# Kernel tuning notes

Measured on AMD Instinct MI355X. Metric: run time of the kernel, lower is better.

## Reference

```python
import jax, jax.numpy as jnp
import numpy as np

BUFFER_C = 1.25

def setup_inputs() -> dict:
    key = jax.random.key(0)
    k1, k2, k3 = jax.random.split(key, 3)
    T, D, E = 4096, 1024, 8
    x = jax.random.normal(k1, (T, D), dtype=jnp.float32)
    Wg = jax.random.normal(k2, (D, E), dtype=jnp.float32) / np.sqrt(D)
    bg = jnp.zeros((E,), dtype=jnp.float32)
    W = jax.random.normal(k3, (E, D, D), dtype=jnp.float32) / np.sqrt(D)
    b = jnp.zeros((E, D), dtype=jnp.float32)
    return {"x": x, "Wg": Wg, "bg": bg, "W": W, "b": b}


def reference(x, Wg, bg, W, b):
    # Top-1 (Switch-style) routing with capacity buffer, per-expert Linear,
    # prob-weighted combine, plus load-balancing aux loss.
    T, D = x.shape
    E = W.shape[0]
    capacity = int(BUFFER_C * T / E)

    logits = x @ Wg + bg                      # [T, E]
    probs = jax.nn.softmax(logits, axis=-1)   # [T, E]
    top_idx = jnp.argmax(probs, axis=-1)      # [T]
    top_prob = jnp.take_along_axis(probs, top_idx[:, None], axis=-1)[:, 0]

    onehot = jax.nn.one_hot(top_idx, E, dtype=x.dtype)       # [T, E]
    # 1-indexed position of each token within its expert's buffer
    pos = jnp.cumsum(onehot, axis=0) * onehot                # [T, E]
    dispatch = jnp.where((onehot > 0) & (pos <= capacity), 1.0, 0.0).astype(x.dtype)

    # dense dispatch/combine equivalent of the masked per-expert loop
    xe = jnp.einsum('te,td->etd', dispatch, x)               # [E, T, D]
    ye = jnp.einsum('etd,edf->etf', xe, W) + b[:, None, :]   # [E, T, D]
    y = jnp.einsum('te,etf->tf', dispatch, ye)               # [T, D] (0 for dropped)
    out = y * top_prob[:, None]

    # aux load-balance loss: E * sum_e f_e * P_e
    f = onehot.mean(axis=0)
    P = probs.mean(axis=0)
    aux_loss = E * jnp.sum(f * P)
    return out, aux_loss
```

## Files before the change

### kernel.cpp

```cpp
#include <hip/hip_runtime.h>
#include <hip/hip_bf16.h>
#include <cstdint>

#define T_TOK 4096
#define D_DIM 1024
#define E_EXP 8
#define CAP   640
#define NBIN  64
#define MAXDROP 3456
#define MT    10

typedef __attribute__((ext_vector_type(8))) short short8;
typedef __attribute__((ext_vector_type(4))) float f32x4;

__device__ inline unsigned short f2bf(float f) {
    uint32_t u = __float_as_uint(f);
    u += 0x7fffu + ((u >> 16) & 1u);
    return (unsigned short)(u >> 16);
}

__device__ inline void dma16(const void* g, void* l) {
    __builtin_amdgcn_global_load_lds(
        (const __attribute__((address_space(1))) unsigned int*)g,
        (__attribute__((address_space(3))) unsigned int*)l, 16, 0, 0);
}

#define WB_TILE(e, nt, kt) ((((size_t)(e) * 16 + (nt)) * 16 + (kt)) * 4096)
#define XG_TILE(e, mt, kt) ((((size_t)(e) * MT + (mt)) * 16 + (kt)) * 4096)

__global__ __launch_bounds__(256) void prep_kernel(
    const float* __restrict__ x, const float* __restrict__ Wg,
    const float* __restrict__ bg, const float* __restrict__ W,
    unsigned short* __restrict__ Wb,
    int* __restrict__ top_idx, float* __restrict__ top_prob, float* __restrict__ ppart)
{
    int bid = blockIdx.x;
    int tid = threadIdx.x;

    if (bid < 2048) {
        __shared__ unsigned short tile[64][66];
        int e  = bid >> 8;
        int kt = (bid >> 4) & 15;
        int nt = bid & 15;
        int k0 = kt * 64, n0 = nt * 64;
        const float* Wsrc = W + (size_t)e * D_DIM * D_DIM;
        #pragma unroll
        for (int p = 0; p < 4; p++) {
            int kk = p * 16 + (tid >> 4);
            int nn = (tid & 15) * 4;
            float4 v = *(const float4*)(Wsrc + (size_t)(k0 + kk) * D_DIM + n0 + nn);
            ushort4 u;
            u.x = f2bf(v.x); u.y = f2bf(v.y); u.z = f2bf(v.z); u.w = f2bf(v.w);
            *(ushort4*)&tile[kk][nn] = u;
        }
        __syncthreads();
        unsigned short* dst = Wb + WB_TILE(e, nt, kt);
        #pragma unroll
        for (int p = 0; p < 2; p++) {
            int c = tid + 256 * p;
            int g = c >> 6, n = c & 63;
            short8 v;
            #pragma unroll
            for (int z = 0; z < 8; z++) v[z] = (short)tile[g * 8 + z][n];
            *(short8*)&dst[(size_t)c * 8] = v;
        }
    } else {
        __shared__ float WgT[8][1024];
        #pragma unroll
        for (int r = 0; r < 4; r++) {
            int d = tid + 256 * r;
            const float4* wr = (const float4*)(Wg + (size_t)d * 8);
            float4 a = wr[0], bq = wr[1];
            WgT[0][d] = a.x;  WgT[1][d] = a.y;  WgT[2][d] = a.z;  WgT[3][d] = a.w;
            WgT[4][d] = bq.x; WgT[5][d] = bq.y; WgT[6][d] = bq.z; WgT[7][d] = bq.w;
        }
        __syncthreads();

        int wid  = tid >> 6;
        int lane = tid & 63;
        int t = (bid - 2048) * 4 + wid;

        const float* xr = x + (size_t)t * D_DIM;

        float acc[8];
        #pragma unroll
        for (int e = 0; e < 8; e++) acc[e] = 0.f;

        #pragma unroll
        for (int ii = 0; ii < 8; ii++) {
            int da = lane + 128 * ii;
            int db = da + 64;
            float xa = xr[da];
            float xc = xr[db];
            #pragma unroll
            for (int e = 0; e < 8; e++)
                acc[e] += xa * WgT[e][da] + xc * WgT[e][db];
        }
        #pragma unroll
        for (int off = 32; off > 0; off >>= 1) {
            #pragma unroll
            for (int e = 0; e < 8; e++) acc[e] += __shfl_xor(acc[e], off, 64);
        }
        if (lane == 0) {
            float lg[8];
            #pragma unroll
            for (int e = 0; e < 8; e++) lg[e] = acc[e] + bg[e];
            float m = lg[0]; int am = 0;
            #pragma unroll
            for (int e = 1; e < 8; e++) { if (lg[e] > m) { m = lg[e]; am = e; } }
            float ex[8], s = 0.f;
            #pragma unroll
            for (int e = 0; e < 8; e++) { ex[e] = expf(lg[e] - m); s += ex[e]; }
            float inv = 1.f / s;
            top_idx[t]  = am;
            top_prob[t] = ex[am] * inv;
            int bin = (int)(bid & (NBIN - 1));
            #pragma unroll
            for (int e = 0; e < 8; e++) atomicAdd(&ppart[bin * 8 + e], ex[e] * inv);
        }
    }
}

__global__ __launch_bounds__(1024) void scan_kernel(
    const int* __restrict__ top_idx,
    int* __restrict__ tok_list, int* __restrict__ cnt,
    const float* __restrict__ ppart,
    float* __restrict__ out, float* __restrict__ out_aux)
{
    __shared__ int counts[64][8];
    __shared__ int excl[64][8];
    __shared__ int fulltot[8];
    __shared__ int droplist[MAXDROP];
    __shared__ int ndrop;

    int tid  = threadIdx.x;
    int wv   = tid >> 6;
    int lane = tid & 63;
    unsigned long long ltmask = (lane == 0) ? 0ull : ((~0ull) >> (64 - lane));

    if (tid == 0) ndrop = 0;

    int ecache[4];
    #pragma unroll
    for (int c = 0; c < 4; c++)
        ecache[c] = top_idx[(4 * wv + c) * 64 + lane];

    #pragma unroll
    for (int c = 0; c < 4; c++) {
        int chunk = 4 * wv + c;
        int e = ecache[c];
        #pragma unroll
        for (int q = 0; q < 8; q++) {
            unsigned long long mk = __ballot(e == q);
            int tot = __popcll(mk);
            if (lane == q) counts[chunk][q] = tot;
        }
    }
    __syncthreads();

    if (wv == 0) {
        #pragma unroll
        for (int q = 0; q < 8; q++) {
            int v = counts[lane][q];
            int orig = v;
            #pragma unroll
            for (int off = 1; off < 64; off <<= 1) {
                int n = __shfl_up(v, off, 64);
                if (lane >= off) v += n;
            }
            excl[lane][q] = v - orig;
            int total = __shfl(v, 63, 64);
            if (lane == 0) {
                fulltot[q] = total;
                cnt[q] = total < CAP ? total : CAP;
            }
        }
    }
    __syncthreads();

    #pragma unroll
    for (int c = 0; c < 4; c++) {
        int chunk = 4 * wv + c;
        int t = chunk * 64 + lane;
        int e = ecache[c];
        int pos = 0;
        #pragma unroll
        for (int q = 0; q < 8; q++) {
            unsigned long long mk = __ballot(e == q);
            if (e == q) pos = excl[chunk][q] + __popcll(mk & ltmask);
        }
        if (pos < CAP) {
            tok_list[e * CAP + pos] = t;
        } else {
            int di = atomicAdd(&ndrop, 1);
            droplist[di] = t;
        }
    }
    __syncthreads();

    int nd = ndrop;
    int grp = tid >> 8;
    int col = (tid & 255) * 4;
    float4 z = {0.f, 0.f, 0.f, 0.f};
    for (int d = grp; d < nd; d += 4) {
        int row = droplist[d];
        *(float4*)&out[(size_t)row * D_DIM + col] = z;
    }

    if (wv == 0) {
        float p[8];
        #pragma unroll
        for (int e = 0; e < 8; e++) p[e] = ppart[lane * 8 + e];
        #pragma unroll
        for (int off = 32; off > 0; off >>= 1) {
            #pragma unroll
            for (int e = 0; e < 8; e++) p[e] += __shfl_xor(p[e], off, 64);
        }
        if (lane == 0) {
            float s = 0.f;
            #pragma unroll
            for (int e = 0; e < 8; e++)
                s += ((float)fulltot[e] / (float)T_TOK) * (p[e] / (float)T_TOK);
            out_aux[0] = (float)E_EXP * s;
        }
    }
}

__global__ __launch_bounds__(256) void gather_kernel(
    const float* __restrict__ x, const int* __restrict__ tok_list,
    const int* __restrict__ cnt, unsigned short* __restrict__ xg)
{
    int bid = blockIdx.x;
    int e   = bid / 40;
    int rem = bid % 40;
    int mt  = rem >> 2, ktg = rem & 3;
    int count = cnt[e];
    int m0 = mt * 64;
    if (m0 >= count) return;

    int tid = threadIdx.x;
    const int* tl = tok_list + e * CAP;

    #pragma unroll
    for (int kk = 0; kk < 4; kk++) {
        int kt = ktg * 4 + kk;
        unsigned short* dst = xg + XG_TILE(e, mt, kt);
        #pragma unroll
        for (int p = 0; p < 2; p++) {
            int c = tid + 256 * p;
            int g = c >> 6, row = c & 63;
            int gm = m0 + row;
            int tok = tl[gm < count ? gm : count - 1];
            const float* src = x + (size_t)tok * D_DIM + kt * 64 + g * 8;
            float4 v0 = *(const float4*)(src);
            float4 v1 = *(const float4*)(src + 4);
            short8 v;
            v[0] = f2bf(v0.x); v[1] = f2bf(v0.y); v[2] = f2bf(v0.z); v[3] = f2bf(v0.w);
            v[4] = f2bf(v1.x); v[5] = f2bf(v1.y); v[6] = f2bf(v1.z); v[7] = f2bf(v1.w);
            *(short8*)&dst[(size_t)c * 8] = v;
        }
    }
}

__device__ inline void stage_dma(const unsigned short* gAt, const unsigned short* gBt,
                                 unsigned short (*Ab)[64][8], unsigned short (*Bb)[64][8],
                                 int w, int lane)
{
    size_t lo = (size_t)lane * 8;
    dma16(gAt + (size_t)w * 512 + lo,       &Ab[w][0][0]);
    dma16(gAt + (size_t)(w + 4) * 512 + lo, &Ab[w + 4][0][0]);
    dma16(gBt + (size_t)w * 512 + lo,       &Bb[w][0][0]);
    dma16(gBt + (size_t)(w + 4) * 512 + lo, &Bb[w + 4][0][0]);
}

__global__ __launch_bounds__(256) void expert_gemm(
    const unsigned short* __restrict__ xg, const unsigned short* __restrict__ Wb,
    const float* __restrict__ bias,
    const int* __restrict__ tok_list, const int* __restrict__ cnt,
    const float* __restrict__ top_prob, float* __restrict__ out)
{
    int bid = blockIdx.x;
    int e   = bid / (MT * 16);
    int rem = bid % (MT * 16);
    int mt  = rem >> 4, nt = rem & 15;
    int count = cnt[e];
    int m0 = mt * 64;
    if (m0 >= count) return;
    int n0 = nt * 64;

    __shared__ unsigned short Ab[2][8][64][8];
    __shared__ unsigned short Bb[2][8][64][8];

    int tid  = threadIdx.x;
    int lane = tid & 63, w = tid >> 6;
    int quad = lane >> 4, l16 = lane & 15;
    int mw = (w >> 1) * 32, nw = (w & 1) * 32;

    const int* tl = tok_list + e * CAP;
    const unsigned short* gA0 = xg + XG_TILE(e, mt, 0);
    const unsigned short* gB0 = Wb + WB_TILE(e, nt, 0);

    f32x4 acc[2][2];
    #pragma unroll
    for (int i = 0; i < 2; i++)
        #pragma unroll
        for (int j = 0; j < 2; j++)
            acc[i][j] = (f32x4){0.f, 0.f, 0.f, 0.f};

    stage_dma(gA0, gB0, Ab[0], Bb[0], w, lane);

    int cur = 0;
    #pragma unroll 1
    for (int kt = 0; kt < 16; kt++) {
        __syncthreads();
        if (kt + 1 < 16)
            stage_dma(gA0 + (size_t)(kt + 1) * 4096, gB0 + (size_t)(kt + 1) * 4096,
                      Ab[cur ^ 1], Bb[cur ^ 1], w, lane);

        short8 af[2][2], bf[2][2];
        #pragma unroll
        for (int s = 0; s < 2; s++) {
            #pragma unroll
            for (int i = 0; i < 2; i++) {
                af[s][i] = *(const short8*)&Ab[cur][s * 4 + quad][mw + 16 * i + l16][0];
                bf[s][i] = *(const short8*)&Bb[cur][s * 4 + quad][nw + 16 * i + l16][0];
            }
        }
        #pragma unroll
        for (int s = 0; s < 2; s++)
            #pragma unroll
            for (int i = 0; i < 2; i++)
                #pragma unroll
                for (int j = 0; j < 2; j++)
                    acc[i][j] = __builtin_amdgcn_mfma_f32_16x16x32_bf16(
                        af[s][i], bf[s][j], acc[i][j], 0, 0, 0);
        cur ^= 1;
    }

    float bv[2];
    #pragma unroll
    for (int j = 0; j < 2; j++)
        bv[j] = bias[e * D_DIM + n0 + nw + 16 * j + l16];

    #pragma unroll
    for (int i = 0; i < 2; i++) {
        int rb = m0 + mw + 16 * i + quad * 4;
        #pragma unroll
        for (int r = 0; r < 4; r++) {
            int gm = rb + r;
            if (gm >= count) continue;
            int tok = tl[gm];
            float p = top_prob[tok];
            float* orow = out + (size_t)tok * D_DIM + n0 + nw + l16;
            #pragma unroll
            for (int j = 0; j < 2; j++)
                orow[16 * j] = (acc[i][j][r] + bv[j]) * p;
        }
    }
}

extern "C" void kernel_launch(void* const* d_in, const int* in_sizes, int n_in,
                              void* d_out, int out_size, void* d_ws, size_t ws_size,
                              hipStream_t stream) {
    const float* x  = (const float*)d_in[0];
    const float* Wg = (const float*)d_in[1];
    const float* bg = (const float*)d_in[2];
    const float* W  = (const float*)d_in[3];
    const float* b  = (const float*)d_in[4];
    float* out = (float*)d_out;

    char* ws = (char*)d_ws;
    unsigned short* Wb = (unsigned short*)(ws + 0);
    unsigned short* xg = (unsigned short*)(ws + 16777216);
    int*   top_idx  = (int*)(ws + 27262976);
    float* top_prob = (float*)(ws + 27279360);
    int*   tok_list = (int*)(ws + 27295744);
    int*   cnt      = (int*)(ws + 27316224);
    float* ppart    = (float*)(ws + 27316256);

    hipMemsetAsync(ppart, 0, NBIN * 8 * sizeof(float), stream);
    hipLaunchKernelGGL(prep_kernel, dim3(2048 + T_TOK / 4), dim3(256), 0, stream,
                       x, Wg, bg, W, Wb, top_idx, top_prob, ppart);
    hipLaunchKernelGGL(scan_kernel, dim3(1), dim3(1024), 0, stream,
                       top_idx, tok_list, cnt, ppart, out, out + (size_t)T_TOK * D_DIM);
    hipLaunchKernelGGL(gather_kernel, dim3(320), dim3(256), 0, stream,
                       x, tok_list, cnt, xg);
    hipLaunchKernelGGL(expert_gemm, dim3(E_EXP * MT * 16), dim3(256), 0, stream,
                       xg, Wb, b, tok_list, cnt, top_prob, out);
}
```

Before: 166.9 us.

## Split prep into transpose and gate kernels, widen GEMM M-tile to 128

The fused prep kernel is split into a weight transpose/convert kernel and a separate gate kernel using 1024-thread blocks. The separate memset is dropped and ppart is zeroed inside the transpose kernel instead. The expert GEMM tile grows from 64x64 to 128x64 so each W tile loaded from memory feeds twice as many rows, halving B traffic. The cost is more accumulators per thread and fewer blocks in the grid. Splitting prep also serializes gating after the transpose, where the two halves previously ran concurrently in one launch.

Result: no change. 167.2 us (+0.2%).

```diff
diff --git a/kernel.cpp b/kernel.cpp
--- a/kernel.cpp
+++ b/kernel.cpp
@@ -28,96 +28,96 @@
 #define WB_TILE(e, nt, kt) ((((size_t)(e) * 16 + (nt)) * 16 + (kt)) * 4096)
 #define XG_TILE(e, mt, kt) ((((size_t)(e) * MT + (mt)) * 16 + (kt)) * 4096)
 
-__global__ __launch_bounds__(256) void prep_kernel(
+__global__ __launch_bounds__(256) void trans_kernel(
+    const float* __restrict__ W, unsigned short* __restrict__ Wb,
+    float* __restrict__ ppart)
+{
+    __shared__ unsigned short tile[64][66];
+    int bid = blockIdx.x, tid = threadIdx.x;
+    if (bid == 0) { ppart[tid] = 0.f; ppart[tid + 256] = 0.f; }
+
+    int e  = bid >> 8;
+    int kt = (bid >> 4) & 15;
+    int nt = bid & 15;
+    int k0 = kt * 64, n0 = nt * 64;
+    const float* Wsrc = W + (size_t)e * D_DIM * D_DIM;
+    #pragma unroll
+    for (int p = 0; p < 4; p++) {
+        int kk = p * 16 + (tid >> 4);
+        int nn = (tid & 15) * 4;
+        float4 v = *(const float4*)(Wsrc + (size_t)(k0 + kk) * D_DIM + n0 + nn);
+        ushort4 u;
+        u.x = f2bf(v.x); u.y = f2bf(v.y); u.z = f2bf(v.z); u.w = f2bf(v.w);
+        *(ushort4*)&tile[kk][nn] = u;
+    }
+    __syncthreads();
+    unsigned short* dst = Wb + WB_TILE(e, nt, kt);
+    #pragma unroll
+    for (int p = 0; p < 2; p++) {
+        int c = tid + 256 * p;
+        int g = c >> 6, n = c & 63;
+        short8 v;
+        #pragma unroll
+        for (int z = 0; z < 8; z++) v[z] = (short)tile[g * 8 + z][n];
+        *(short8*)&dst[(size_t)c * 8] = v;
+    }
+}
+
+__global__ __launch_bounds__(1024) void gate_kernel(
     const float* __restrict__ x, const float* __restrict__ Wg,
-    const float* __restrict__ bg, const float* __restrict__ W,
-    unsigned short* __restrict__ Wb,
+    const float* __restrict__ bg,
     int* __restrict__ top_idx, float* __restrict__ top_prob, float* __restrict__ ppart)
 {
-    int bid = blockIdx.x;
+    __shared__ float WgT[8][1024];
     int tid = threadIdx.x;
-
-    if (bid < 2048) {
-        __shared__ unsigned short tile[64][66];
-        int e  = bid >> 8;
-        int kt = (bid >> 4) & 15;
-        int nt = bid & 15;
-        int k0 = kt * 64, n0 = nt * 64;
-        const float* Wsrc = W + (size_t)e * D_DIM * D_DIM;
-        #pragma unroll
-        for (int p = 0; p < 4; p++) {
-            int kk = p * 16 + (tid >> 4);
-            int nn = (tid & 15) * 4;
-            float4 v = *(const float4*)(Wsrc + (size_t)(k0 + kk) * D_DIM + n0 + nn);
-            ushort4 u;
-            u.x = f2bf(v.x); u.y = f2bf(v.y); u.z = f2bf(v.z); u.w = f2bf(v.w);
-            *(ushort4*)&tile[kk][nn] = u;
-        }
-        __syncthreads();
-        unsigned short* dst = Wb + WB_TILE(e, nt, kt);
-        #pragma unroll
-        for (int p = 0; p < 2; p++) {
-            int c = tid + 256 * p;
-            int g = c >> 6, n = c & 63;
-            short8 v;
-            #pragma unroll
-            for (int z = 0; z < 8; z++) v[z] = (short)tile[g * 8 + z][n];
-            *(short8*)&dst[(size_t)c * 8] = v;
-        }
-    } else {
-        __shared__ float WgT[8][1024];
-        #pragma unroll
-        for (int r = 0; r < 4; r++) {
-            int d = tid + 256 * r;
-            const float4* wr = (const float4*)(Wg + (size_t)d * 8);
-            float4 a = wr[0], bq = wr[1];
-            WgT[0][d] = a.x;  WgT[1][d] = a.y;  WgT[2][d] = a.z;  WgT[3][d] = a.w;
-            WgT[4][d] = bq.x; WgT[5][d] = bq.y; WgT[6][d] = bq.z; WgT[7][d] = bq.w;
-        }
-        __syncthreads();
-
-        int wid  = tid >> 6;
-        int lane = tid & 63;
-        int t = (bid - 2048) * 4 + wid;
-
-        const float* xr = x + (size_t)t * D_DIM;
-
-        float acc[8];
-        #pragma unroll
-        for (int e = 0; e < 8; e++) acc[e] = 0.f;
-
-        #pragma unroll
-        for (int ii = 0; ii < 8; ii++) {
-            int da = lane + 128 * ii;
-            int db = da + 64;
-            float xa = xr[da];
-            float xc = xr[db];
-            #pragma unroll
-            for (int e = 0; e < 8; e++)
-                acc[e] += xa * WgT[e][da] + xc * WgT[e][db];
-        }
-        #pragma unroll
-        for (int off = 32; off > 0; off >>= 1) {
-            #pragma unroll
-            for (int e = 0; e < 8; e++) acc[e] += __shfl_xor(acc[e], off, 64);
-        }
-        if (lane == 0) {
-            float lg[8];
-            #pragma unroll
-            for (int e = 0; e < 8; e++) lg[e] = acc[e] + bg[e];
-            float m = lg[0]; int am = 0;
-            #pragma unroll
-            for (int e = 1; e < 8; e++) { if (lg[e] > m) { m = lg[e]; am = e; } }
-            float ex[8], s = 0.f;
-            #pragma unroll
-            for (int e = 0; e < 8; e++) { ex[e] = expf(lg[e] - m); s += ex[e]; }
-            float inv = 1.f / s;
-            top_idx[t]  = am;
-            top_prob[t] = ex[am] * inv;
-            int bin = (int)(bid & (NBIN - 1));
-            #pragma unroll
-            for (int e = 0; e < 8; e++) atomicAdd(&ppart[bin * 8 + e], ex[e] * inv);
-        }
+    {
+        const float4* wr = (const float4*)(Wg + (size_t)tid * 8);
+        float4 a = wr[0], bq = wr[1];
+        WgT[0][tid] = a.x;  WgT[1][tid] = a.y;  WgT[2][tid] = a.z;  WgT[3][tid] = a.w;
+        WgT[4][tid] = bq.x; WgT[5][tid] = bq.y; WgT[6][tid] = bq.z; WgT[7][tid] = bq.w;
+    }
+    __syncthreads();
+
+    int wid  = tid >> 6;
+    int lane = tid & 63;
+    int t = blockIdx.x * 16 + wid;
+
+    const float* xr = x + (size_t)t * D_DIM;
+    float acc[8];
+    #pragma unroll
+    for (int e = 0; e < 8; e++) acc[e] = 0.f;
+
+    #pragma unroll
+    for (int ii = 0; ii < 8; ii++) {
+        int da = lane + 128 * ii;
+        int db = da + 64;
+        float xa = xr[da];
+        float xc = xr[db];
+        #pragma unroll
+        for (int e = 0; e < 8; e++)
+            acc[e] += xa * WgT[e][da] + xc * WgT[e][db];
+    }
+    #pragma unroll
+    for (int off = 32; off > 0; off >>= 1) {
+        #pragma unroll
+        for (int e = 0; e < 8; e++) acc[e] += __shfl_xor(acc[e], off, 64);
+    }
+    if (lane == 0) {
+        float lg[8];
+        #pragma unroll
+        for (int e = 0; e < 8; e++) lg[e] = acc[e] + bg[e];
+        float m = lg[0]; int am = 0;
+        #pragma unroll
+        for (int e = 1; e < 8; e++) { if (lg[e] > m) { m = lg[e]; am = e; } }
+        float ex[8], s = 0.f;
+        #pragma unroll
+        for (int e = 0; e < 8; e++) { ex[e] = expf(lg[e] - m); s += ex[e]; }
+        float inv = 1.f / s;
+        top_idx[t]  = am;
+        top_prob[t] = ex[am] * inv;
+        int bin = (int)(blockIdx.x & (NBIN - 1));
+        #pragma unroll
+        for (int e = 0; e < 8; e++) atomicAdd(&ppart[bin * 8 + e], ex[e] * inv);
     }
 }
 
@@ -262,17 +262,6 @@
     }
 }
 
-__device__ inline void stage_dma(const unsigned short* gAt, const unsigned short* gBt,
-                                 unsigned short (*Ab)[64][8], unsigned short (*Bb)[64][8],
-                                 int w, int lane)
-{
-    size_t lo = (size_t)lane * 8;
-    dma16(gAt + (size_t)w * 512 + lo,       &Ab[w][0][0]);
-    dma16(gAt + (size_t)(w + 4) * 512 + lo, &Ab[w + 4][0][0]);
-    dma16(gBt + (size_t)w * 512 + lo,       &Bb[w][0][0]);
-    dma16(gBt + (size_t)(w + 4) * 512 + lo, &Bb[w + 4][0][0]);
-}
-
 __global__ __launch_bounds__(256) void expert_gemm(
     const unsigned short* __restrict__ xg, const unsigned short* __restrict__ Wb,
     const float* __restrict__ bias,
@@ -280,56 +269,71 @@
     const float* __restrict__ top_prob, float* __restrict__ out)
 {
     int bid = blockIdx.x;
-    int e   = bid / (MT * 16);
-    int rem = bid % (MT * 16);
-    int mt  = rem >> 4, nt = rem & 15;
+    int e   = bid / 80;
+    int rem = bid % 80;
+    int mtt = rem >> 4, nt = rem & 15;
     int count = cnt[e];
-    int m0 = mt * 64;
+    int m0 = mtt * 128;
     if (m0 >= count) return;
     int n0 = nt * 64;
 
-    __shared__ unsigned short Ab[2][8][64][8];
+    __shared__ unsigned short Ab[2][2][8][64][8];
     __shared__ unsigned short Bb[2][8][64][8];
 
     int tid  = threadIdx.x;
     int lane = tid & 63, w = tid >> 6;
     int quad = lane >> 4, l16 = lane & 15;
-    int mw = (w >> 1) * 32, nw = (w & 1) * 32;
+    int mh = w >> 1;
+    int nw = (w & 1) * 32;
+    size_t lo = (size_t)lane * 8;
 
     const int* tl = tok_list + e * CAP;
-    const unsigned short* gA0 = xg + XG_TILE(e, mt, 0);
-    const unsigned short* gB0 = Wb + WB_TILE(e, nt, 0);
-
-    f32x4 acc[2][2];
-    #pragma unroll
-    for (int i = 0; i < 2; i++)
+    const unsigned short* A0 = xg + XG_TILE(e, mtt * 2, 0) + lo;
+    const unsigned short* A1 = xg + XG_TILE(e, mtt * 2 + 1, 0) + lo;
+    const unsigned short* B0 = Wb + WB_TILE(e, nt, 0) + lo;
+
+    f32x4 acc[4][2];
+    #pragma unroll
+    for (int i = 0; i < 4; i++)
         #pragma unroll
         for (int j = 0; j < 2; j++)
             acc[i][j] = (f32x4){0.f, 0.f, 0.f, 0.f};
 
-    stage_dma(gA0, gB0, Ab[0], Bb[0], w, lane);
-
+    auto stage = [&](int kt, int buf) {
+        const unsigned short* a0 = A0 + (size_t)kt * 4096;
+        const unsigned short* a1 = A1 + (size_t)kt * 4096;
+        const unsigned short* bb = B0 + (size_t)kt * 4096;
+        #pragma unroll
+        for (int d = 0; d < 6; d++) {
+            int g = w + 4 * d;
+            if (g < 8)        dma16(a0 + (size_t)g * 512,        &Ab[buf][0][g][0][0]);
+            else if (g < 16)  dma16(a1 + (size_t)(g - 8) * 512,  &Ab[buf][1][g - 8][0][0]);
+            else              dma16(bb + (size_t)(g - 16) * 512, &Bb[buf][g - 16][0][0]);
+        }
+    };
+
+    stage(0, 0);
     int cur = 0;
     #pragma unroll 1
     for (int kt = 0; kt < 16; kt++) {
         __syncthreads();
-        if (kt + 1 < 16)
-            stage_dma(gA0 + (size_t)(kt + 1) * 4096, gB0 + (size_t)(kt + 1) * 4096,
-                      Ab[cur ^ 1], Bb[cur ^ 1], w, lane);
-
-        short8 af[2][2], bf[2][2];
+        if (kt + 1 < 16) stage(kt + 1, cur ^ 1);
+
+        short8 af[2][4], bf[2][2];
         #pragma unroll
         for (int s = 0; s < 2; s++) {
-            #pragma unroll
-            for (int i = 0; i < 2; i++) {
-                af[s][i] = *(const short8*)&Ab[cur][s * 4 + quad][mw + 16 * i + l16][0];
-                bf[s][i] = *(const short8*)&Bb[cur][s * 4 + quad][nw + 16 * i + l16][0];
-            }
+            int g = s * 4 + quad;
+            #pragma unroll
+            for (int i = 0; i < 4; i++)
+                af[s][i] = *(const short8*)&Ab[cur][mh][g][16 * i + l16][0];
+            #pragma unroll
+            for (int j = 0; j < 2; j++)
+                bf[s][j] = *(const short8*)&Bb[cur][g][nw + 16 * j + l16][0];
         }
         #pragma unroll
         for (int s = 0; s < 2; s++)
             #pragma unroll
-            for (int i = 0; i < 2; i++)
+            for (int i = 0; i < 4; i++)
                 #pragma unroll
                 for (int j = 0; j < 2; j++)
                     acc[i][j] = __builtin_amdgcn_mfma_f32_16x16x32_bf16(
@@ -343,8 +347,8 @@
         bv[j] = bias[e * D_DIM + n0 + nw + 16 * j + l16];
 
     #pragma unroll
-    for (int i = 0; i < 2; i++) {
-        int rb = m0 + mw + 16 * i + quad * 4;
+    for (int i = 0; i < 4; i++) {
+        int rb = m0 + mh * 64 + 16 * i + quad * 4;
         #pragma unroll
         for (int r = 0; r < 4; r++) {
             int gm = rb + r;
@@ -378,13 +382,13 @@
     int*   cnt      = (int*)(ws + 27316224);
     float* ppart    = (float*)(ws + 27316256);
 
-    hipMemsetAsync(ppart, 0, NBIN * 8 * sizeof(float), stream);
-    hipLaunchKernelGGL(prep_kernel, dim3(2048 + T_TOK / 4), dim3(256), 0, stream,
-                       x, Wg, bg, W, Wb, top_idx, top_prob, ppart);
+    hipLaunchKernelGGL(trans_kernel, dim3(2048), dim3(256), 0, stream, W, Wb, ppart);
+    hipLaunchKernelGGL(gate_kernel, dim3(T_TOK / 16), dim3(1024), 0, stream,
+                       x, Wg, bg, top_idx, top_prob, ppart);
     hipLaunchKernelGGL(scan_kernel, dim3(1), dim3(1024), 0, stream,
                        top_idx, tok_list, cnt, ppart, out, out + (size_t)T_TOK * D_DIM);
     hipLaunchKernelGGL(gather_kernel, dim3(320), dim3(256), 0, stream,
                        x, tok_list, cnt, xg);
-    hipLaunchKernelGGL(expert_gemm, dim3(E_EXP * MT * 16), dim3(256), 0, stream,
+    hipLaunchKernelGGL(expert_gemm, dim3(E_EXP * 5 * 16), dim3(256), 0, stream,
                        xg, Wb, b, tok_list, cnt, top_prob, out);
 }
```
